# Performance work log

Measured on AMD Instinct MI355X. Metric: run time of the kernel, lower is better.

## Reference

```python
import jax, jax.numpy as jnp
import numpy as np

N_NODES = 50000
N_EDGES = 800000
IN_DIM = 128
NUM_GRAPHS = 64
NEG_SLOPE = 0.2  # PyG GATConv default


def _gat_layer(x, src, dst, W, a_s, a_d, b):
    """PyG GATConv (concat=True), eval mode (no dropout).
    x: [N, Fin]; W: [H*C, Fin]; a_s, a_d: [H, C]; b: [H*C]."""
    N = x.shape[0]
    H, C = a_s.shape
    h = (x @ W.T).reshape(N, H, C)                      # [N,H,C]
    es = jnp.einsum('nhc,hc->nh', h, a_s)               # [N,H]
    ed = jnp.einsum('nhc,hc->nh', h, a_d)               # [N,H]
    e = jax.nn.leaky_relu(es[src] + ed[dst], NEG_SLOPE)  # [E,H]
    # segment softmax over incoming edges of each destination node
    m = jax.ops.segment_max(e, dst, num_segments=N)     # [N,H]
    ex = jnp.exp(e - m[dst])
    denom = jax.ops.segment_sum(ex, dst, num_segments=N)
    alpha = ex / denom[dst]                             # [E,H]
    out = jax.ops.segment_sum(h[src] * alpha[:, :, None], dst, num_segments=N)
    return out.reshape(N, H * C) + b


def _make_params(key):
    dims = [(512, IN_DIM, 8, 64), (256, 512, 8, 32), (128, 256, 8, 16), (512, 128, 8, 64)]
    ps = {}
    k = key
    for i, (out_f, in_f, H, C) in enumerate(dims, 1):
        k, k1, k2, k3 = jax.random.split(k, 4)
        s = 1.0 / np.sqrt(in_f)
        ps[f'W{i}'] = jax.random.normal(k1, (out_f, in_f), jnp.float32) * s
        ps[f'a{i}s'] = jax.random.normal(k2, (H, C), jnp.float32) * 0.1
        ps[f'a{i}d'] = jax.random.normal(k3, (H, C), jnp.float32) * 0.1
        ps[f'b{i}'] = jnp.zeros((out_f,), jnp.float32)
    k, k1, k2 = jax.random.split(k, 3)
    ps['lw1'] = jax.random.normal(k1, (32, 512), jnp.float32) * (1.0 / np.sqrt(512))
    ps['lb1'] = jnp.zeros((32,), jnp.float32)
    ps['lw2'] = jax.random.normal(k2, (2, 32), jnp.float32) * (1.0 / np.sqrt(32))
    ps['lb2'] = jnp.zeros((2,), jnp.float32)
    return ps


def setup_inputs() -> dict:
    key = jax.random.key(0)
    kx, ke, kb, kp = jax.random.split(key, 4)
    x = jax.random.normal(kx, (N_NODES, IN_DIM), jnp.float32)
    edge_index = jax.random.randint(ke, (2, N_EDGES), 0, N_NODES, jnp.int64 if jax.config.jax_enable_x64 else jnp.int32)
    batch = jnp.sort(jax.random.randint(kb, (N_NODES,), 0, NUM_GRAPHS, edge_index.dtype))
    inp = {'x': x, 'edge_index': edge_index, 'batch': batch}
    inp.update(_make_params(kp))
    return inp


def reference(x, edge_index, batch,
              W1, a1s, a1d, b1, W2, a2s, a2d, b2,
              W3, a3s, a3d, b3, W4, a4s, a4d, b4,
              lw1, lb1, lw2, lb2):
    N = x.shape[0]
    # PyG GATConv add_self_loops=True
    loop = jnp.arange(N, dtype=edge_index.dtype)
    src = jnp.concatenate([edge_index[0], loop])
    dst = jnp.concatenate([edge_index[1], loop])

    h = jax.nn.elu(_gat_layer(x, src, dst, W1, a1s, a1d, b1))
    h = jax.nn.elu(_gat_layer(h, src, dst, W2, a2s, a2d, b2))
    h = jax.nn.elu(_gat_layer(h, src, dst, W3, a3s, a3d, b3))
    h = _gat_layer(h, src, dst, W4, a4s, a4d, b4)

    # global mean pool over graphs
    sums = jax.ops.segment_sum(h, batch, num_segments=NUM_GRAPHS)
    cnts = jax.ops.segment_sum(jnp.ones((N, 1), h.dtype), batch, num_segments=NUM_GRAPHS)
    g = sums / jnp.maximum(cnts, 1.0)                   # [G, 512]

    g = jax.nn.elu(g @ lw1.T + lb1)                     # dropout skipped (eval)
    return g @ lw2.T + lb2                              # [G, 2]
```

## Files before the change

### kernel.cpp

```cpp
#include <hip/hip_runtime.h>
#include <math.h>

#define NN 50000
#define NE 800000
#define NEP (NE + NN)
#define NGR 64
#define NHEAD 8
#define MPAD 50048
#define KSTASH 6

typedef short short8 __attribute__((ext_vector_type(8)));
typedef float floatx4 __attribute__((ext_vector_type(4)));
typedef unsigned uintx4 __attribute__((ext_vector_type(4)));

__device__ inline float bf2f(short s) {
    union { unsigned u; float f; } v;
    v.u = ((unsigned)(unsigned short)s) << 16;
    return v.f;
}
__device__ inline float bf2f_lo(unsigned p) {
    union { unsigned u; float f; } v; v.u = p << 16; return v.f;
}
__device__ inline float bf2f_hi(unsigned p) {
    union { unsigned u; float f; } v; v.u = p & 0xffff0000u; return v.f;
}
__device__ inline short f2bf(float f) {
    union { float f; unsigned u; } v; v.f = f;
    unsigned r = v.u + 0x7fffu + ((v.u >> 16) & 1u);
    return (short)(r >> 16);
}

__device__ inline void gl_lds16(const short* g, short* l) {
    __builtin_amdgcn_global_load_lds(
        (const __attribute__((address_space(1))) unsigned int*)g,
        (__attribute__((address_space(3))) unsigned int*)l, 16, 0, 0);
}

__global__ void count_deg(const int* __restrict__ ei, int* __restrict__ deg) {
    int e = blockIdx.x * 256 + threadIdx.x;
    if (e >= NEP) return;
    int d = (e < NE) ? ei[NE + e] : (e - NE);
    atomicAdd(&deg[d], 1);
}

__global__ __launch_bounds__(1024) void scan_local(const int* __restrict__ deg,
                                                   int* __restrict__ out,
                                                   int* __restrict__ bsum, int n) {
    __shared__ int sd[1024];
    int b = blockIdx.x, t = threadIdx.x;
    int i = b * 1024 + t;
    int v = (i < n) ? deg[i] : 0;
    sd[t] = v;
    __syncthreads();
    for (int off = 1; off < 1024; off <<= 1) {
        int tmp = (t >= off) ? sd[t - off] : 0;
        __syncthreads();
        sd[t] += tmp;
        __syncthreads();
    }
    if (i < n) out[i] = sd[t] - v;
    if (t == 1023) bsum[b] = sd[1023];
}

__global__ void scan_bsum(int* __restrict__ bsum, int nb) {
    if (threadIdx.x == 0) {
        int s = 0;
        for (int i = 0; i < nb; i++) { int v = bsum[i]; bsum[i] = s; s += v; }
        bsum[nb] = s;
    }
}

__global__ void scan_add(int* __restrict__ row_ptr, int* __restrict__ cursor,
                         const int* __restrict__ bsum, int n, int nb) {
    int i = blockIdx.x * 256 + threadIdx.x;
    if (i < n) {
        int v = row_ptr[i] + bsum[i >> 10];
        row_ptr[i] = v;
        cursor[i] = v;
    } else if (i == n) {
        row_ptr[n] = bsum[nb];
    }
}

__global__ void scatter_edges(const int* __restrict__ ei, int* __restrict__ cursor,
                              int* __restrict__ srcs) {
    int e = blockIdx.x * 256 + threadIdx.x;
    if (e >= NEP) return;
    int s, d;
    if (e < NE) { s = ei[e]; d = ei[NE + e]; }
    else        { s = e - NE; d = e - NE; }
    int pos = atomicAdd(&cursor[d], 1);
    srcs[pos] = s;
}

__global__ void conv_w_all(const float* __restrict__ w0, const float* __restrict__ w1,
                           const float* __restrict__ w2, const float* __restrict__ w3,
                           short* __restrict__ out) {
    int i = blockIdx.x * 256 + threadIdx.x;
    if (i >= 294912) return;
    const float* src; int off;
    if (i < 65536)       { src = w0; off = i; }
    else if (i < 196608) { src = w1; off = i - 65536; }
    else if (i < 229376) { src = w2; off = i - 196608; }
    else                 { src = w3; off = i - 229376; }
    out[i] = f2bf(src[off]);
}

__global__ void conv_x_pad4(const float* __restrict__ x, short* __restrict__ xb) {
    int i = blockIdx.x * 256 + threadIdx.x;
    if (i >= MPAD * 32) return;
    int r = i >> 5;
    short4 o;
    if (r < NN) {
        float4 v = *(const float4*)&x[(size_t)i * 4];
        o.x = f2bf(v.x); o.y = f2bf(v.y); o.z = f2bf(v.z); o.w = f2bf(v.w);
    } else {
        o.x = o.y = o.z = o.w = 0;
    }
    *(short4*)&xb[(size_t)i * 4] = o;
}

template <int C>
__global__ __launch_bounds__(256) void gemm_bf(const short* __restrict__ A,
                                               const short* __restrict__ B,
                                               short* __restrict__ Cout,
                                               const float* __restrict__ a_s,
                                               const float* __restrict__ a_d,
                                               float* __restrict__ es,
                                               float* __restrict__ ed,
                                               int K) {
    constexpr int Nc = 8 * C;
    constexpr int colTiles = Nc / 128;
    constexpr int JPH = C / 16;
    constexpr int HPW = 64 / C;
    __shared__ __align__(16) short As[128 * 64];
    __shared__ __align__(16) short Bs[128 * 64];
    int bx = blockIdx.x % colTiles;
    int by = blockIdx.x / colTiles;
    int row0 = by * 128, col0 = bx * 128;
    int t = threadIdx.x;
    int lane = t & 63, w = t >> 6;
    int wr = (w >> 1) * 64, wc = (w & 1) * 64;
    int lrow = lane & 15, lq = lane >> 4;

    int srow = lane >> 3;
    int kcsrc = (lane & 7) ^ srow;

    floatx4 acc[4][4];
#pragma unroll
    for (int i = 0; i < 4; i++)
#pragma unroll
        for (int j = 0; j < 4; j++) acc[i][j] = (floatx4)0.0f;

    for (int k0 = 0; k0 < K; k0 += 64) {
#pragma unroll
        for (int it = 0; it < 4; it++) {
            int r0 = w * 32 + it * 8;
            int r = r0 + srow;
            gl_lds16(&A[(size_t)(row0 + r) * K + k0 + kcsrc * 8], &As[r0 * 64]);
            gl_lds16(&B[(size_t)(col0 + r) * K + k0 + kcsrc * 8], &Bs[r0 * 64]);
        }
        __syncthreads();
#pragma unroll
        for (int kk = 0; kk < 2; kk++) {
            int slot = (kk * 4 + lq) ^ (lrow & 7);
            short8 af[4], bfr[4];
#pragma unroll
            for (int i = 0; i < 4; i++)
                af[i] = *(const short8*)&As[(wr + i * 16 + lrow) * 64 + slot * 8];
#pragma unroll
            for (int j = 0; j < 4; j++)
                bfr[j] = *(const short8*)&Bs[(wc + j * 16 + lrow) * 64 + slot * 8];
#pragma unroll
            for (int i = 0; i < 4; i++)
#pragma unroll
                for (int j = 0; j < 4; j++)
                    acc[i][j] = __builtin_amdgcn_mfma_f32_16x16x32_bf16(af[i], bfr[j], acc[i][j], 0, 0, 0);
        }
        __syncthreads();
    }

#pragma unroll
    for (int i = 0; i < 4; i++)
#pragma unroll
        for (int j = 0; j < 4; j++)
#pragma unroll
            for (int r = 0; r < 4; r++) {
                int row = row0 + wr + i * 16 + lq * 4 + r;
                int col = col0 + wc + j * 16 + lrow;
                Cout[(size_t)row * Nc + col] = f2bf(acc[i][j][r]);
            }

    float asv[4], adv[4];
#pragma unroll
    for (int j = 0; j < 4; j++) {
        int colA = col0 + wc + j * 16 + lrow;
        asv[j] = a_s[colA];
        adv[j] = a_d[colA];
    }
    int hb = (col0 + wc) / C;
#pragma unroll
    for (int i = 0; i < 4; i++)
#pragma unroll
        for (int r = 0; r < 4; r++) {
            float s_h[HPW], d_h[HPW];
#pragma unroll
            for (int hh = 0; hh < HPW; hh++) { s_h[hh] = 0.f; d_h[hh] = 0.f; }
#pragma unroll
            for (int j = 0; j < 4; j++) {
                s_h[j / JPH] = fmaf(acc[i][j][r], asv[j], s_h[j / JPH]);
                d_h[j / JPH] = fmaf(acc[i][j][r], adv[j], d_h[j / JPH]);
            }
#pragma unroll
            for (int hh = 0; hh < HPW; hh++) {
#pragma unroll
                for (int off = 1; off <= 8; off <<= 1) {
                    s_h[hh] += __shfl_xor(s_h[hh], off);
                    d_h[hh] += __shfl_xor(d_h[hh], off);
                }
            }
            if (lrow == 0) {
                int row = row0 + wr + i * 16 + lq * 4 + r;
                if (row < NN) {
#pragma unroll
                    for (int hh = 0; hh < HPW; hh++) {
                        es[row * 8 + hb + hh] = s_h[hh];
                        ed[row * 8 + hb + hh] = d_h[hh];
                    }
                }
            }
        }
}

__global__ __launch_bounds__(256) void alpha_kernel(const float* __restrict__ es,
                                                    const float* __restrict__ ed,
                                                    const int* __restrict__ row_ptr,
                                                    const int* __restrict__ srcs,
                                                    float* __restrict__ alpha) {
    int wave = threadIdx.x >> 6, lane = threadIdx.x & 63;
    int n = __builtin_amdgcn_readfirstlane(blockIdx.x * 4 + wave);
    int start = row_ptr[n];
    int deg = row_ptr[n + 1] - start;
    int m8 = deg * 8;
    const int* sp = srcs + start;
    float* ap = alpha + start;
    int hh = lane & 7;
    int hoff = hh * NEP;
    float edv = ed[n * 8 + hh];
    float st[KSTASH];
    float pm = -1e30f, ps = 0.f;
#pragma unroll
    for (int i = 0; i < KSTASH; i++) {
        int idx = lane + i * 64;
        if (idx < m8) {
            int s = sp[idx >> 3];
            float e = es[s * 8 + hh] + edv;
            e = e > 0.f ? e : 0.2f * e;
            st[i] = e;
            float mn = fmaxf(pm, e);
            ps = ps * __expf(pm - mn) + __expf(e - mn);
            pm = mn;
        }
    }
    for (int idx = lane + KSTASH * 64; idx < m8; idx += 64) {
        int s = sp[idx >> 3];
        float e = es[s * 8 + hh] + edv;
        e = e > 0.f ? e : 0.2f * e;
        float mn = fmaxf(pm, e);
        ps = ps * __expf(pm - mn) + __expf(e - mn);
        pm = mn;
    }
#pragma unroll
    for (int off = 8; off <= 32; off <<= 1) {
        float mo = __shfl_xor(pm, off);
        float so = __shfl_xor(ps, off);
        float mn = fmaxf(pm, mo);
        ps = ps * __expf(pm - mn) + so * __expf(mo - mn);
        pm = mn;
    }
    float invd = 1.0f / ps;
#pragma unroll
    for (int i = 0; i < KSTASH; i++) {
        int idx = lane + i * 64;
        if (idx < m8) ap[hoff + (idx >> 3)] = __expf(st[i] - pm) * invd;
    }
    for (int idx = lane + KSTASH * 64; idx < m8; idx += 64) {
        int s = sp[idx >> 3];
        float e = es[s * 8 + hh] + edv;
        e = e > 0.f ? e : 0.2f * e;
        ap[hoff + (idx >> 3)] = __expf(e - pm) * invd;
    }
}

template <int C, bool ELU>
__global__ __launch_bounds__(256) void aggr_npg(const short* __restrict__ h,
                                                const float* __restrict__ alpha,
                                                const int* __restrict__ row_ptr,
                                                const int* __restrict__ srcs,
                                                const float* __restrict__ bias,
                                                short* __restrict__ out) {
    constexpr int HC = NHEAD * C;
    constexpr int NCH = HC / 64;
    constexpr int RSH = (C == 64) ? 10 : (C == 32) ? 9 : 8;
    int chunk = blockIdx.x % NCH;
    int grp   = blockIdx.x / NCH;
    int lane = threadIdx.x & 63;
    int wave = threadIdx.x >> 6;
    int sub = lane & 7;
    int g   = lane >> 3;
    int n = grp * 32 + wave * 8 + g;
    int c0 = chunk * 64 + sub * 8;
    unsigned c02 = (unsigned)(c0 * 2);
    int head = c0 / C;
    bool valid = n < NN;
    int start = 0, deg = 0;
    if (valid) {
        start = row_ptr[n];
        deg = row_ptr[n + 1] - start;
    }
    unsigned soff = (unsigned)start;
    unsigned aoff = (unsigned)(head * NEP + start);
    float acc[8];
#pragma unroll
    for (int j = 0; j < 8; j++) acc[j] = 0.f;
    int k = 0;
    for (; k + 1 < deg; k += 2) {
        int s0 = srcs[soff + k];
        int s1 = srcs[soff + k + 1];
        float w0 = alpha[aoff + k];
        float w1 = alpha[aoff + k + 1];
        uintx4 h0 = *(const uintx4*)((const char*)h + (((unsigned)s0 << RSH) + c02));
        uintx4 h1 = *(const uintx4*)((const char*)h + (((unsigned)s1 << RSH) + c02));
#pragma unroll
        for (int j = 0; j < 4; j++) {
            acc[2 * j]     = fmaf(w0, bf2f_lo(h0[j]), acc[2 * j]);
            acc[2 * j + 1] = fmaf(w0, bf2f_hi(h0[j]), acc[2 * j + 1]);
        }
#pragma unroll
        for (int j = 0; j < 4; j++) {
            acc[2 * j]     = fmaf(w1, bf2f_lo(h1[j]), acc[2 * j]);
            acc[2 * j + 1] = fmaf(w1, bf2f_hi(h1[j]), acc[2 * j + 1]);
        }
    }
    if (k < deg) {
        int s0 = srcs[soff + k];
        float w0 = alpha[aoff + k];
        uintx4 h0 = *(const uintx4*)((const char*)h + (((unsigned)s0 << RSH) + c02));
#pragma unroll
        for (int j = 0; j < 4; j++) {
            acc[2 * j]     = fmaf(w0, bf2f_lo(h0[j]), acc[2 * j]);
            acc[2 * j + 1] = fmaf(w0, bf2f_hi(h0[j]), acc[2 * j + 1]);
        }
    }
    if (valid) {
        floatx4 b0 = *(const floatx4*)&bias[c0];
        floatx4 b1 = *(const floatx4*)&bias[c0 + 4];
        float bb[8] = {b0[0], b0[1], b0[2], b0[3], b1[0], b1[1], b1[2], b1[3]};
        unsigned pk[4];
#pragma unroll
        for (int j = 0; j < 4; j++) {
            float o0 = acc[2 * j] + bb[2 * j];
            float o1 = acc[2 * j + 1] + bb[2 * j + 1];
            if (ELU) {
                o0 = o0 > 0.f ? o0 : (__expf(o0) - 1.0f);
                o1 = o1 > 0.f ? o1 : (__expf(o1) - 1.0f);
            }
            pk[j] = ((unsigned)(unsigned short)f2bf(o0)) |
                    (((unsigned)(unsigned short)f2bf(o1)) << 16);
        }
        *(uintx4*)&out[(size_t)n * HC + c0] = *(uintx4*)pk;
    }
}

__global__ __launch_bounds__(256) void pool_kernel(const short* __restrict__ h,
                                                   const int* __restrict__ batch,
                                                   float* __restrict__ gout) {
    __shared__ float red[4 * 64];
    int g = blockIdx.x >> 3;
    int fc = (blockIdx.x & 7) * 64;
    int lo = 0, hi = NN;
    while (lo < hi) { int mid = (lo + hi) >> 1; if (batch[mid] < g) lo = mid + 1; else hi = mid; }
    int s = lo;
    lo = 0; hi = NN;
    while (lo < hi) { int mid = (lo + hi) >> 1; if (batch[mid] < g + 1) lo = mid + 1; else hi = mid; }
    int e = lo;
    int t = threadIdx.x;
    int wave = t >> 6, lane = t & 63;
    int f8 = (lane & 7) * 8;
    int stripe = wave * 8 + (lane >> 3);
    float acc[8];
#pragma unroll
    for (int j = 0; j < 8; j++) acc[j] = 0.f;
    for (int r = s + stripe; r < e; r += 32) {
        short8 v = *(const short8*)&h[(size_t)r * 512 + fc + f8];
#pragma unroll
        for (int j = 0; j < 8; j++) acc[j] += bf2f(v[j]);
    }
#pragma unroll
    for (int j = 0; j < 8; j++) {
        acc[j] += __shfl_xor(acc[j], 8);
        acc[j] += __shfl_xor(acc[j], 16);
        acc[j] += __shfl_xor(acc[j], 32);
    }
    if (lane < 8) {
#pragma unroll
        for (int j = 0; j < 8; j++) red[wave * 64 + lane * 8 + j] = acc[j];
    }
    __syncthreads();
    if (t < 64) {
        float v = red[t] + red[64 + t] + red[128 + t] + red[192 + t];
        float inv = 1.0f / fmaxf((float)(e - s), 1.0f);
        gout[g * 512 + fc + t] = v * inv;
    }
}

__global__ __launch_bounds__(64) void mlp_kernel(const float* __restrict__ g,
                                                 const float* __restrict__ lw1,
                                                 const float* __restrict__ lb1,
                                                 const float* __restrict__ lw2,
                                                 const float* __restrict__ lb2,
                                                 float* __restrict__ outp) {
    __shared__ float gv[512];
    __shared__ float y1[32];
    int b = blockIdx.x, t = threadIdx.x;
    for (int i = t; i < 512; i += 64) gv[i] = g[b * 512 + i];
    __syncthreads();
    if (t < 32) {
        float a = lb1[t];
        for (int k = 0; k < 512; k++) a = fmaf(gv[k], lw1[t * 512 + k], a);
        y1[t] = a > 0.f ? a : (__expf(a) - 1.0f);
    }
    __syncthreads();
    if (t < 2) {
        float a = lb2[t];
        for (int k = 0; k < 32; k++) a = fmaf(y1[k], lw2[t * 32 + k], a);
        outp[b * 2 + t] = a;
    }
}

extern "C" void kernel_launch(void* const* d_in, const int* in_sizes, int n_in,
                              void* d_out, int out_size, void* d_ws, size_t ws_size,
                              hipStream_t stream) {
    (void)in_sizes; (void)n_in; (void)out_size; (void)ws_size;
    const float* x     = (const float*)d_in[0];
    const int*   ei    = (const int*)d_in[1];
    const int*   batch = (const int*)d_in[2];
    const float* W[4]  = {(const float*)d_in[3], (const float*)d_in[7],
                          (const float*)d_in[11], (const float*)d_in[15]};
    const float* As_[4] = {(const float*)d_in[4], (const float*)d_in[8],
                           (const float*)d_in[12], (const float*)d_in[16]};
    const float* Ad_[4] = {(const float*)d_in[5], (const float*)d_in[9],
                           (const float*)d_in[13], (const float*)d_in[17]};
    const float* Bi[4]  = {(const float*)d_in[6], (const float*)d_in[10],
                           (const float*)d_in[14], (const float*)d_in[18]};
    const float* lw1 = (const float*)d_in[19];
    const float* lb1 = (const float*)d_in[20];
    const float* lw2 = (const float*)d_in[21];
    const float* lb2 = (const float*)d_in[22];
    float* out = (float*)d_out;

    short* Ab = (short*)d_ws;
    short* Hb = Ab + (size_t)MPAD * 512;
    short* Wb = Hb + (size_t)MPAD * 512;
    short* Wb_[4] = {Wb, Wb + 65536, Wb + 196608, Wb + 229376};
    float* esb  = (float*)(Wb + 294912);
    float* edb  = esb + NN * NHEAD;
    float* gbuf = edb + NN * NHEAD;
    int* row_ptr = (int*)(gbuf + NGR * 512);
    int* cursor  = row_ptr + (NN + 1);
    int* srcs    = cursor + (NN + 1);
    int* bsum    = srcs + NEP;
    float* alphab = (float*)(bsum + 64);

    const int nblk = (NN + 1023) / 1024;

    hipMemsetAsync(cursor, 0, NN * sizeof(int), stream);
    count_deg<<<(NEP + 255) / 256, 256, 0, stream>>>(ei, cursor);
    scan_local<<<nblk, 1024, 0, stream>>>(cursor, row_ptr, bsum, NN);
    scan_bsum<<<1, 64, 0, stream>>>(bsum, nblk);
    scan_add<<<(NN + 256) / 256, 256, 0, stream>>>(row_ptr, cursor, bsum, NN, nblk);
    scatter_edges<<<(NEP + 255) / 256, 256, 0, stream>>>(ei, cursor, srcs);

    conv_x_pad4<<<(MPAD * 32 + 255) / 256, 256, 0, stream>>>(x, Ab);
    conv_w_all<<<(294912 + 255) / 256, 256, 0, stream>>>(W[0], W[1], W[2], W[3], Wb);

    const int rowTiles = MPAD / 128;
    const int ag  = NN / 4;
    const int ngb = (NN + 31) / 32;

    gemm_bf<64><<<rowTiles * 4, 256, 0, stream>>>(Ab, Wb_[0], Hb, As_[0], Ad_[0], esb, edb, 128);
    alpha_kernel<<<ag, 256, 0, stream>>>(esb, edb, row_ptr, srcs, alphab);
    aggr_npg<64, true><<<ngb * 8, 256, 0, stream>>>(Hb, alphab, row_ptr, srcs, Bi[0], Ab);

    gemm_bf<32><<<rowTiles * 2, 256, 0, stream>>>(Ab, Wb_[1], Hb, As_[1], Ad_[1], esb, edb, 512);
    alpha_kernel<<<ag, 256, 0, stream>>>(esb, edb, row_ptr, srcs, alphab);
    aggr_npg<32, true><<<ngb * 4, 256, 0, stream>>>(Hb, alphab, row_ptr, srcs, Bi[1], Ab);

    gemm_bf<16><<<rowTiles * 1, 256, 0, stream>>>(Ab, Wb_[2], Hb, As_[2], Ad_[2], esb, edb, 256);
    alpha_kernel<<<ag, 256, 0, stream>>>(esb, edb, row_ptr, srcs, alphab);
    aggr_npg<16, true><<<ngb * 2, 256, 0, stream>>>(Hb, alphab, row_ptr, srcs, Bi[2], Ab);

    gemm_bf<64><<<rowTiles * 4, 256, 0, stream>>>(Ab, Wb_[3], Hb, As_[3], Ad_[3], esb, edb, 128);
    alpha_kernel<<<ag, 256, 0, stream>>>(esb, edb, row_ptr, srcs, alphab);
    aggr_npg<64, false><<<ngb * 8, 256, 0, stream>>>(Hb, alphab, row_ptr, srcs, Bi[3], Ab);

    pool_kernel<<<NGR * 8, 256, 0, stream>>>(Ab, batch, gbuf);
    mlp_kernel<<<NGR, 64, 0, stream>>>(gbuf, lw1, lb1, lw2, lb2, out);
}
```

Before: 776.2 us.

## Pad CSR rows to multiples of four and unroll aggregation by four

After: 761.5 us. About the same (-1.9%).

```diff
diff --git a/kernel.cpp b/kernel.cpp
--- a/kernel.cpp
+++ b/kernel.cpp
@@ -4,6 +4,7 @@
 #define NN 50000
 #define NE 800000
 #define NEP (NE + NN)
+#define NEPP 1000000
 #define NGR 64
 #define NHEAD 8
 #define MPAD 50048
@@ -49,7 +50,7 @@
     __shared__ int sd[1024];
     int b = blockIdx.x, t = threadIdx.x;
     int i = b * 1024 + t;
-    int v = (i < n) ? deg[i] : 0;
+    int v = (i < n) ? ((deg[i] + 3) & ~3) : 0;
     sd[t] = v;
     __syncthreads();
     for (int off = 1; off < 1024; off <<= 1) {
@@ -235,17 +236,18 @@
 __global__ __launch_bounds__(256) void alpha_kernel(const float* __restrict__ es,
                                                     const float* __restrict__ ed,
                                                     const int* __restrict__ row_ptr,
+                                                    const int* __restrict__ degr,
                                                     const int* __restrict__ srcs,
                                                     float* __restrict__ alpha) {
     int wave = threadIdx.x >> 6, lane = threadIdx.x & 63;
     int n = __builtin_amdgcn_readfirstlane(blockIdx.x * 4 + wave);
     int start = row_ptr[n];
-    int deg = row_ptr[n + 1] - start;
+    int degp = row_ptr[n + 1] - start;
+    int deg = degr[n];
     int m8 = deg * 8;
+    int mp8 = degp * 8;
     const int* sp = srcs + start;
-    float* ap = alpha + start;
     int hh = lane & 7;
-    int hoff = hh * NEP;
     float edv = ed[n * 8 + hh];
     float st[KSTASH];
     float pm = -1e30f, ps = 0.f;
@@ -279,17 +281,20 @@
         pm = mn;
     }
     float invd = 1.0f / ps;
+    int hoff = hh * NEPP;
 #pragma unroll
     for (int i = 0; i < KSTASH; i++) {
         int idx = lane + i * 64;
-        if (idx < m8) ap[hoff + (idx >> 3)] = __expf(st[i] - pm) * invd;
+        if (idx < m8) alpha[hoff + start + (idx >> 3)] = __expf(st[i] - pm) * invd;
     }
     for (int idx = lane + KSTASH * 64; idx < m8; idx += 64) {
         int s = sp[idx >> 3];
         float e = es[s * 8 + hh] + edv;
         e = e > 0.f ? e : 0.2f * e;
-        ap[hoff + (idx >> 3)] = __expf(e - pm) * invd;
-    }
+        alpha[hoff + start + (idx >> 3)] = __expf(e - pm) * invd;
+    }
+    for (int idx = m8 + lane; idx < mp8; idx += 64)
+        alpha[(size_t)(idx & 7) * NEPP + start + (idx >> 3)] = 0.f;
 }
 
 template <int C, bool ELU>
@@ -313,24 +318,29 @@
     unsigned c02 = (unsigned)(c0 * 2);
     int head = c0 / C;
     bool valid = n < NN;
-    int start = 0, deg = 0;
+    int start = 0, degp = 0;
     if (valid) {
         start = row_ptr[n];
-        deg = row_ptr[n + 1] - start;
+        degp = row_ptr[n + 1] - start;
     }
     unsigned soff = (unsigned)start;
-    unsigned aoff = (unsigned)(head * NEP + start);
+    unsigned aoff = (unsigned)(head * NEPP + start);
     float acc[8];
 #pragma unroll
     for (int j = 0; j < 8; j++) acc[j] = 0.f;
-    int k = 0;
-    for (; k + 1 < deg; k += 2) {
+    for (int k = 0; k < degp; k += 4) {
         int s0 = srcs[soff + k];
         int s1 = srcs[soff + k + 1];
+        int s2 = srcs[soff + k + 2];
+        int s3 = srcs[soff + k + 3];
         float w0 = alpha[aoff + k];
         float w1 = alpha[aoff + k + 1];
+        float w2 = alpha[aoff + k + 2];
+        float w3 = alpha[aoff + k + 3];
         uintx4 h0 = *(const uintx4*)((const char*)h + (((unsigned)s0 << RSH) + c02));
         uintx4 h1 = *(const uintx4*)((const char*)h + (((unsigned)s1 << RSH) + c02));
+        uintx4 h2 = *(const uintx4*)((const char*)h + (((unsigned)s2 << RSH) + c02));
+        uintx4 h3 = *(const uintx4*)((const char*)h + (((unsigned)s3 << RSH) + c02));
 #pragma unroll
         for (int j = 0; j < 4; j++) {
             acc[2 * j]     = fmaf(w0, bf2f_lo(h0[j]), acc[2 * j]);
@@ -341,15 +351,15 @@
             acc[2 * j]     = fmaf(w1, bf2f_lo(h1[j]), acc[2 * j]);
             acc[2 * j + 1] = fmaf(w1, bf2f_hi(h1[j]), acc[2 * j + 1]);
         }
-    }
-    if (k < deg) {
-        int s0 = srcs[soff + k];
-        float w0 = alpha[aoff + k];
-        uintx4 h0 = *(const uintx4*)((const char*)h + (((unsigned)s0 << RSH) + c02));
 #pragma unroll
         for (int j = 0; j < 4; j++) {
-            acc[2 * j]     = fmaf(w0, bf2f_lo(h0[j]), acc[2 * j]);
-            acc[2 * j + 1] = fmaf(w0, bf2f_hi(h0[j]), acc[2 * j + 1]);
+            acc[2 * j]     = fmaf(w2, bf2f_lo(h2[j]), acc[2 * j]);
+            acc[2 * j + 1] = fmaf(w2, bf2f_hi(h2[j]), acc[2 * j + 1]);
+        }
+#pragma unroll
+        for (int j = 0; j < 4; j++) {
+            acc[2 * j]     = fmaf(w3, bf2f_lo(h3[j]), acc[2 * j]);
+            acc[2 * j + 1] = fmaf(w3, bf2f_hi(h3[j]), acc[2 * j + 1]);
         }
     }
     if (valid) {
@@ -468,17 +478,19 @@
     float* gbuf = edb + NN * NHEAD;
     int* row_ptr = (int*)(gbuf + NGR * 512);
     int* cursor  = row_ptr + (NN + 1);
-    int* srcs    = cursor + (NN + 1);
-    int* bsum    = srcs + NEP;
+    int* degr    = cursor + (NN + 1);
+    int* srcs    = degr + NN;
+    int* bsum    = srcs + NEPP;
     float* alphab = (float*)(bsum + 64);
 
     const int nblk = (NN + 1023) / 1024;
 
-    hipMemsetAsync(cursor, 0, NN * sizeof(int), stream);
-    count_deg<<<(NEP + 255) / 256, 256, 0, stream>>>(ei, cursor);
-    scan_local<<<nblk, 1024, 0, stream>>>(cursor, row_ptr, bsum, NN);
+    hipMemsetAsync(degr, 0, NN * sizeof(int), stream);
+    count_deg<<<(NEP + 255) / 256, 256, 0, stream>>>(ei, degr);
+    scan_local<<<nblk, 1024, 0, stream>>>(degr, row_ptr, bsum, NN);
     scan_bsum<<<1, 64, 0, stream>>>(bsum, nblk);
     scan_add<<<(NN + 256) / 256, 256, 0, stream>>>(row_ptr, cursor, bsum, NN, nblk);
+    hipMemsetAsync(srcs, 0, NEPP * sizeof(int), stream);
     scatter_edges<<<(NEP + 255) / 256, 256, 0, stream>>>(ei, cursor, srcs);
 
     conv_x_pad4<<<(MPAD * 32 + 255) / 256, 256, 0, stream>>>(x, Ab);
@@ -489,19 +501,19 @@
     const int ngb = (NN + 31) / 32;
 
     gemm_bf<64><<<rowTiles * 4, 256, 0, stream>>>(Ab, Wb_[0], Hb, As_[0], Ad_[0], esb, edb, 128);
-    alpha_kernel<<<ag, 256, 0, stream>>>(esb, edb, row_ptr, srcs, alphab);
+    alpha_kernel<<<ag, 256, 0, stream>>>(esb, edb, row_ptr, degr, srcs, alphab);
     aggr_npg<64, true><<<ngb * 8, 256, 0, stream>>>(Hb, alphab, row_ptr, srcs, Bi[0], Ab);
 
     gemm_bf<32><<<rowTiles * 2, 256, 0, stream>>>(Ab, Wb_[1], Hb, As_[1], Ad_[1], esb, edb, 512);
-    alpha_kernel<<<ag, 256, 0, stream>>>(esb, edb, row_ptr, srcs, alphab);
+    alpha_kernel<<<ag, 256, 0, stream>>>(esb, edb, row_ptr, degr, srcs, alphab);
     aggr_npg<32, true><<<ngb * 4, 256, 0, stream>>>(Hb, alphab, row_ptr, srcs, Bi[1], Ab);
 
     gemm_bf<16><<<rowTiles * 1, 256, 0, stream>>>(Ab, Wb_[2], Hb, As_[2], Ad_[2], esb, edb, 256);
-    alpha_kernel<<<ag, 256, 0, stream>>>(esb, edb, row_ptr, srcs, alphab);
+    alpha_kernel<<<ag, 256, 0, stream>>>(esb, edb, row_ptr, degr, srcs, alphab);
     aggr_npg<16, true><<<ngb * 2, 256, 0, stream>>>(Hb, alphab, row_ptr, srcs, Bi[2], Ab);
 
     gemm_bf<64><<<rowTiles * 4, 256, 0, stream>>>(Ab, Wb_[3], Hb, As_[3], Ad_[3], esb, edb, 128);
-    alpha_kernel<<<ag, 256, 0, stream>>>(esb, edb, row_ptr, srcs, alphab);
+    alpha_kernel<<<ag, 256, 0, stream>>>(esb, edb, row_ptr, degr, srcs, alphab);
     aggr_npg<64, false><<<ngb * 8, 256, 0, stream>>>(Hb, alphab, row_ptr, srcs, Bi[3], Ab);
 
     pool_kernel<<<NGR * 8, 256, 0, stream>>>(Ab, batch, gbuf);
```
